# Kernel tuning notes

Measured on AMD Instinct MI355X. Metric: run time of the kernel, lower is better.

The kernel has to match this reference:

```python
import jax, jax.numpy as jnp
import numpy as np

RADIUS = 0.08
NSAMPLE = 32


def setup_inputs() -> dict:
    key = jax.random.key(0)
    k1, k2, k3 = jax.random.split(key, 3)
    xyz = jax.random.uniform(k1, (20000, 3), dtype=jnp.float32)          # (N, 3)
    new_xyz = jax.random.uniform(k2, (2, 2048, 3), dtype=jnp.float32)    # (B, P, 3)
    features = jax.random.normal(k3, (64, 20000), dtype=jnp.float32)     # (C, N)
    return {"xyz": xyz, "new_xyz": new_xyz, "features": features}


def _ball_query(xyz, new_xyz, radius, nsample):
    """Replicates pointnet2 grid ball query.
    Returns idx (B,P,nsample) int32 of the FIRST nsample in-ball point indices
    (in original point order), padded with the first found index (0 if none),
    and idn (B,P,nsample) int32 validity flags (all ones if ball is empty,
    matching the kernel's untouched init of 1).
    """
    xyz = jax.lax.stop_gradient(xyz)
    new_xyz = jax.lax.stop_gradient(new_xyz)
    N = xyz.shape[0]
    # squared distances (B, P, N) via ||a||^2 + ||b||^2 - 2 a.b (no (B,P,N,3) temp)
    x2 = jnp.sum(xyz * xyz, axis=-1)                 # (N,)
    q2 = jnp.sum(new_xyz * new_xyz, axis=-1)         # (B, P)
    cross = jnp.einsum("bpd,nd->bpn", new_xyz, xyz)  # (B, P, N)
    d2 = q2[..., None] + x2[None, None, :] - 2.0 * cross
    mask = d2 < radius * radius                      # (B, P, N)
    # encode "first nsample in-ball indices in ascending point order":
    scores = jnp.where(mask, jnp.arange(N, dtype=jnp.int32), N)
    neg_vals, _ = jax.lax.top_k(-scores, nsample)    # largest of -scores = smallest scores
    cand = -neg_vals                                 # (B, P, nsample), sorted ascending
    valid = cand < N
    first = jnp.where(valid[..., :1], cand[..., :1], 0)
    idx = jnp.where(valid, cand, first).astype(jnp.int32)
    empty = ~valid[..., :1]                          # ball has no neighbors
    idn = jnp.where(valid | empty, 1, 0).astype(jnp.int32)
    return idx, idn


def _group(features, idx):
    """features (C, N), idx (B, P, S) -> (B, C, P, S) gather."""
    g = jnp.take(features, idx, axis=1)              # (C, B, P, S)
    return jnp.transpose(g, (1, 0, 2, 3))


def reference(xyz, new_xyz, features):
    idx, idn = _ball_query(xyz, new_xyz, RADIUS, NSAMPLE)
    grouped_xyz = _group(jnp.transpose(xyz), idx)                    # (B, 3, P, S)
    grouped_xyz = grouped_xyz - jnp.transpose(new_xyz, (0, 2, 1))[..., None]
    grouped_features = _group(features, idx)                         # (B, C, P, S)
    new_features = jnp.concatenate([grouped_xyz, grouped_features], axis=1)
    return new_features, idn
```

## Files before the change

### kernel.cpp

```cpp
#include <hip/hip_runtime.h>
#include <hip/hip_bf16.h>

#define NPTS   20000
#define BATCH  2
#define NQ     2048
#define NS     32
#define NC     64
#define NCOUT  67
#define NQTOT  (BATCH * NQ)
#define NF_ELEMS (BATCH * NCOUT * NQ * NS)

#define GRID   12
#define NCELL  (GRID * GRID * GRID)
#define CAND_CAP 128

__device__ __forceinline__ float sq3(float a, float b, float c) {
    return __fadd_rn(__fadd_rn(__fmul_rn(a, a), __fmul_rn(b, b)), __fmul_rn(c, c));
}

__global__ __launch_bounds__(256) void zero_counts_kernel(int* __restrict__ cnt) {
    const int t = threadIdx.x;
    #pragma unroll
    for (int i = 0; i < 7; ++i) {
        const int c = t * 7 + i;
        if (c < NCELL) cnt[c] = 0;
    }
}

__global__ __launch_bounds__(256) void cell_count_kernel(
        const float* __restrict__ xyz, int* __restrict__ cellOf,
        int* __restrict__ cnt) {
    const int n = blockIdx.x * 256 + threadIdx.x;
    if (n >= NPTS) return;
    const float x = xyz[n * 3 + 0];
    const float y = xyz[n * 3 + 1];
    const float z = xyz[n * 3 + 2];
    const int cx = min(max((int)(x * (float)GRID), 0), GRID - 1);
    const int cy = min(max((int)(y * (float)GRID), 0), GRID - 1);
    const int cz = min(max((int)(z * (float)GRID), 0), GRID - 1);
    const int cell = (cx * GRID + cy) * GRID + cz;
    cellOf[n] = cell;
    atomicAdd(&cnt[cell], 1);
}

__global__ __launch_bounds__(256) void scan_kernel(
        const int* __restrict__ cnt, int* __restrict__ start,
        int* __restrict__ cursor) {
    __shared__ int s[256];
    const int t = threadIdx.x;
    int loc[7];
    int sum = 0;
    #pragma unroll
    for (int i = 0; i < 7; ++i) {
        const int c = t * 7 + i;
        const int v = (c < NCELL) ? cnt[c] : 0;
        loc[i] = sum;
        sum += v;
    }
    s[t] = sum;
    __syncthreads();
    for (int off = 1; off < 256; off <<= 1) {
        const int v = (t >= off) ? s[t - off] : 0;
        __syncthreads();
        s[t] += v;
        __syncthreads();
    }
    const int excl = s[t] - sum;
    #pragma unroll
    for (int i = 0; i < 7; ++i) {
        const int c = t * 7 + i;
        if (c < NCELL) {
            const int val = excl + loc[i];
            start[c]  = val;
            cursor[c] = val;
        }
    }
    if (t == 255) start[NCELL] = s[255];
}

__global__ __launch_bounds__(256) void scatter_kernel(
        const float* __restrict__ xyz, const int* __restrict__ cellOf,
        int* __restrict__ cursor, float4* __restrict__ packed) {
    const int n = blockIdx.x * 256 + threadIdx.x;
    if (n >= NPTS) return;
    const int pos = atomicAdd(&cursor[cellOf[n]], 1);
    packed[pos] = make_float4(xyz[n * 3 + 0], xyz[n * 3 + 1], xyz[n * 3 + 2],
                              __int_as_float(n));
}

__device__ __forceinline__ void ce_shfl(int& r0, int& r1, int j,
                                        bool asc0, bool asc1, int lane) {
    const int o0 = __shfl_xor(r0, j);
    const int o1 = __shfl_xor(r1, j);
    const bool lower = (lane & j) == 0;
    r0 = (lower == asc0) ? min(r0, o0) : max(r0, o0);
    r1 = (lower == asc1) ? min(r1, o1) : max(r1, o1);
}

__global__ __launch_bounds__(256) void grid_query_kernel(
        const float4* __restrict__ packed,
        const int*    __restrict__ cellStart,
        const float*  __restrict__ new_xyz,
        int*   __restrict__ idxOut,
        float* __restrict__ idnOut) {
    const float R2 = (float)(0.08 * 0.08);

    const int wid  = threadIdx.x >> 6;
    const int lane = threadIdx.x & 63;
    const int q    = blockIdx.x * 4 + wid;

    __shared__ int cand[4][CAND_CAP];

    const float qx = new_xyz[q * 3 + 0];
    const float qy = new_xyz[q * 3 + 1];
    const float qz = new_xyz[q * 3 + 2];
    const float q2 = sq3(qx, qy, qz);

    const int cx = min(max((int)(qx * (float)GRID), 0), GRID - 1);
    const int cy = min(max((int)(qy * (float)GRID), 0), GRID - 1);
    const int cz = min(max((int)(qz * (float)GRID), 0), GRID - 1);

    const int xlo = max(cx - 1, 0), xhi = min(cx + 1, GRID - 1);
    const int ylo = max(cy - 1, 0), yhi = min(cy + 1, GRID - 1);
    const int zlo = max(cz - 1, 0), zhi = min(cz + 1, GRID - 1);

    const unsigned long long lt = (1ull << lane) - 1ull;
    int cnt = 0;

    for (int dx = xlo; dx <= xhi; ++dx) {
        for (int dy = ylo; dy <= yhi; ++dy) {
            const int row = (dx * GRID + dy) * GRID;
            const int s0 = cellStart[row + zlo];
            const int s1 = cellStart[row + zhi + 1];
            for (int base = s0; base < s1; base += 64) {
                const int i = base + lane;
                bool inball = false;
                int  pid = 0;
                if (i < s1) {
                    const float4 p = packed[i];
                    pid = __float_as_int(p.w);
                    const float x2 = sq3(p.x, p.y, p.z);
                    const float cross = __fadd_rn(
                        __fadd_rn(__fmul_rn(qx, p.x), __fmul_rn(qy, p.y)),
                        __fmul_rn(qz, p.z));
                    const float d2 = __fsub_rn(__fadd_rn(q2, x2),
                                               __fmul_rn(2.0f, cross));
                    inball = d2 < R2;
                }
                const unsigned long long m = __ballot(inball);
                if (inball) {
                    const int pos = cnt + __popcll(m & lt);
                    if (pos < CAND_CAP) cand[wid][pos] = pid;
                }
                cnt += __popcll(m);
            }
        }
    }

    __threadfence_block();

    const int M = min(cnt, CAND_CAP);
    int r0 = (lane      < M) ? cand[wid][lane]      : 0x7fffffff;
    int r1 = (lane + 64 < M) ? cand[wid][lane + 64] : 0x7fffffff;

    #pragma unroll
    for (int k = 2; k <= 64; k <<= 1) {
        #pragma unroll
        for (int j = k >> 1; j >= 1; j >>= 1) {
            const bool asc0 = ((lane & k) == 0);
            const bool asc1 = (((lane | 64) & k) == 0);
            ce_shfl(r0, r1, j, asc0, asc1, lane);
        }
    }
    { const int lo = min(r0, r1), hi = max(r0, r1); r0 = lo; r1 = hi; }
    #pragma unroll
    for (int j = 32; j >= 1; j >>= 1) ce_shfl(r0, r1, j, true, true, lane);

    const int nf = min(cnt, NS);
    const int first = __shfl(r0, 0);
    if (lane < NS) {
        int v; float fl;
        if (cnt == 0) { v = 0; fl = 1.0f; }
        else { v = (lane < nf) ? r0 : first; fl = (lane < nf) ? 1.0f : 0.0f; }
        idxOut[q * NS + lane] = v;
        idnOut[q * NS + lane] = fl;
    }
}

__global__ __launch_bounds__(256) void ball_query_kernel(
        const float* __restrict__ xyz, const float* __restrict__ new_xyz,
        int* __restrict__ idxOut, float* __restrict__ idnOut) {
    const float R2 = (float)(0.08 * 0.08);
    const int wid  = threadIdx.x >> 6;
    const int lane = threadIdx.x & 63;
    const int q    = blockIdx.x * 4 + wid;
    __shared__ int buf[4][NS];
    const float qx = new_xyz[q * 3 + 0];
    const float qy = new_xyz[q * 3 + 1];
    const float qz = new_xyz[q * 3 + 2];
    const float q2 = sq3(qx, qy, qz);
    int cnt = 0;
    for (int base = 0; base < NPTS; base += 64) {
        const int i = base + lane;
        bool inball = false;
        if (i < NPTS) {
            const float px = xyz[i * 3 + 0], py = xyz[i * 3 + 1], pz = xyz[i * 3 + 2];
            const float x2 = sq3(px, py, pz);
            const float cross = __fadd_rn(
                __fadd_rn(__fmul_rn(qx, px), __fmul_rn(qy, py)), __fmul_rn(qz, pz));
            const float d2 = __fsub_rn(__fadd_rn(q2, x2), __fmul_rn(2.0f, cross));
            inball = d2 < R2;
        }
        const unsigned long long m = __ballot(inball);
        if (inball) {
            const int pos = cnt + __popcll(m & ((1ull << lane) - 1ull));
            if (pos < NS) buf[wid][pos] = i;
        }
        cnt += __popcll(m);
        if (cnt >= NS) break;
    }
    __syncthreads();
    if (lane < NS) {
        const int nf = (cnt < NS) ? cnt : NS;
        int v; float fl;
        if (nf == 0) { v = 0; fl = 1.0f; }
        else { v = (lane < nf) ? buf[wid][lane] : buf[wid][0];
               fl = (lane < nf) ? 1.0f : 0.0f; }
        idxOut[q * NS + lane] = v;
        idnOut[q * NS + lane] = fl;
    }
}

__global__ void feat_transpose_kernel(const float* __restrict__ features,
                                      float* __restrict__ featT) {
    __shared__ float tile[64][65];
    const int n0 = blockIdx.x * 64;
    const int t  = threadIdx.x;
    const int nn   = t & 63;
    const int cgrp = t >> 6;
    for (int k = 0; k < 16; ++k) {
        const int cc = cgrp * 16 + k;
        const int n  = n0 + nn;
        if (n < NPTS) tile[cc][nn] = features[cc * NPTS + n];
    }
    __syncthreads();
    const int cc2  = t & 63;
    const int ngrp = t >> 6;
    for (int k = 0; k < 16; ++k) {
        const int nn2 = ngrp * 16 + k;
        const int n   = n0 + nn2;
        if (n < NPTS) featT[n * NC + cc2] = tile[cc2][nn2];
    }
}

__global__ __launch_bounds__(256) void group_kernel(
        const float* __restrict__ xyz,
        const float* __restrict__ new_xyz,
        const float* __restrict__ features,
        const float* __restrict__ featT,
        const int*   __restrict__ idx,
        float* __restrict__ out,
        int haveFeatT) {
    const int q = blockIdx.x;
    const int b = q >> 11;
    const int p = q & (NQ - 1);

    __shared__ int   sidx[NS];
    __shared__ float sq[3];

    const int t = threadIdx.x;
    if (t < NS) sidx[t] = idx[q * NS + t];
    if (t < 3)  sq[t]   = new_xyz[q * 3 + t];
    __syncthreads();

    if (t < 96) {
        const int d = t >> 5;
        const int s = t & 31;
        const int id = sidx[s];
        const int o = ((b * NCOUT + d) * NQ + p) * NS + s;
        out[o] = __fsub_rn(xyz[id * 3 + d], sq[d]);
    }

    const int s  = t & 31;
    const int c4 = t >> 5;
    const int id = sidx[s];
    const int CH_STRIDE = NQ * NS;

    if (haveFeatT) {
        const float4* ft = (const float4*)featT;
        #pragma unroll
        for (int h = 0; h < 2; ++h) {
            const int cc4 = c4 + h * 8;
            const float4 v = ft[id * (NC / 4) + cc4];
            const int cbase = cc4 * 4;
            const int o = ((b * NCOUT + 3 + cbase) * NQ + p) * NS + s;
            out[o]                 = v.x;
            out[o + 1 * CH_STRIDE] = v.y;
            out[o + 2 * CH_STRIDE] = v.z;
            out[o + 3 * CH_STRIDE] = v.w;
        }
    } else {
        #pragma unroll
        for (int h = 0; h < 2; ++h) {
            const int cbase = (c4 + h * 8) * 4;
            #pragma unroll
            for (int k = 0; k < 4; ++k) {
                const int c = cbase + k;
                const int o = ((b * NCOUT + 3 + c) * NQ + p) * NS + s;
                out[o] = features[c * NPTS + id];
            }
        }
    }
}

extern "C" void kernel_launch(void* const* d_in, const int* in_sizes, int n_in,
                              void* d_out, int out_size, void* d_ws, size_t ws_size,
                              hipStream_t stream) {
    const float* xyz      = (const float*)d_in[0];
    const float* new_xyz  = (const float*)d_in[1];
    const float* features = (const float*)d_in[2];

    float* out     = (float*)d_out;
    float* idn_out = out + NF_ELEMS;

    const size_t OFF_IDX    = 0;
    const size_t OFF_FEATT  = 524288;
    const size_t OFF_CNT    = 5644288;
    const size_t OFF_START  = 5651456;
    const size_t OFF_CURSOR = 5658624;
    const size_t OFF_CELLOF = 5665792;
    const size_t OFF_PACKED = 5745792;
    const size_t GRID_TOTAL = 6065792;
    const size_t FEATT_END  = 5644288;

    int*    d_idx    = (int*)((char*)d_ws + OFF_IDX);
    float*  d_featT  = (float*)((char*)d_ws + OFF_FEATT);
    int*    d_cnt    = (int*)((char*)d_ws + OFF_CNT);
    int*    d_start  = (int*)((char*)d_ws + OFF_START);
    int*    d_cursor = (int*)((char*)d_ws + OFF_CURSOR);
    int*    d_cellOf = (int*)((char*)d_ws + OFF_CELLOF);
    float4* d_packed = (float4*)((char*)d_ws + OFF_PACKED);

    const int haveGrid  = (ws_size >= GRID_TOTAL) ? 1 : 0;
    const int haveFeatT = (ws_size >= FEATT_END) ? 1 : 0;

    if (haveFeatT) {
        feat_transpose_kernel<<<(NPTS + 63) / 64, 256, 0, stream>>>(features, d_featT);
    }

    if (haveGrid) {
        zero_counts_kernel<<<1, 256, 0, stream>>>(d_cnt);
        cell_count_kernel<<<(NPTS + 255) / 256, 256, 0, stream>>>(xyz, d_cellOf, d_cnt);
        scan_kernel<<<1, 256, 0, stream>>>(d_cnt, d_start, d_cursor);
        scatter_kernel<<<(NPTS + 255) / 256, 256, 0, stream>>>(xyz, d_cellOf, d_cursor, d_packed);
        grid_query_kernel<<<NQTOT / 4, 256, 0, stream>>>(d_packed, d_start, new_xyz,
                                                         d_idx, idn_out);
    } else {
        ball_query_kernel<<<NQTOT / 4, 256, 0, stream>>>(xyz, new_xyz, d_idx, idn_out);
    }

    group_kernel<<<NQTOT, 256, 0, stream>>>(xyz, new_xyz, features,
                                            haveFeatT ? d_featT : nullptr,
                                            d_idx, out, haveFeatT);
}
```

Before: 107.1 us.

## Fuse grid query with grouping and feature transpose with cell counting

Merges the feature transpose into the cell-count kernel, and merges the grouping gather into the grid query kernel so that neighbor indices stay in shared memory instead of going through global memory. This cuts two kernel launches and the idx round trip. The brute-force and no-workspace fallbacks are removed, so the code now assumes the workspace is large enough. Grouping now runs with one wave per query instead of a 256-thread block per query, which lowers parallelism in the output-write phase.

Measured after the change: 99.98 us. -6.6%, faster.

```diff
diff --git a/kernel.cpp b/kernel.cpp
--- a/kernel.cpp
+++ b/kernel.cpp
@@ -27,20 +27,44 @@
     }
 }
 
-__global__ __launch_bounds__(256) void cell_count_kernel(
-        const float* __restrict__ xyz, int* __restrict__ cellOf,
+__global__ __launch_bounds__(256) void transpose_count_kernel(
+        const float* __restrict__ features, const float* __restrict__ xyz,
+        float* __restrict__ featT, int* __restrict__ cellOf,
         int* __restrict__ cnt) {
-    const int n = blockIdx.x * 256 + threadIdx.x;
-    if (n >= NPTS) return;
-    const float x = xyz[n * 3 + 0];
-    const float y = xyz[n * 3 + 1];
-    const float z = xyz[n * 3 + 2];
-    const int cx = min(max((int)(x * (float)GRID), 0), GRID - 1);
-    const int cy = min(max((int)(y * (float)GRID), 0), GRID - 1);
-    const int cz = min(max((int)(z * (float)GRID), 0), GRID - 1);
-    const int cell = (cx * GRID + cy) * GRID + cz;
-    cellOf[n] = cell;
-    atomicAdd(&cnt[cell], 1);
+    __shared__ float tile[64][65];
+    const int n0 = blockIdx.x * 64;
+    const int t  = threadIdx.x;
+
+    if (t < 64) {
+        const int n = n0 + t;
+        if (n < NPTS) {
+            const float x = xyz[n * 3 + 0];
+            const float y = xyz[n * 3 + 1];
+            const float z = xyz[n * 3 + 2];
+            const int cx = min(max((int)(x * (float)GRID), 0), GRID - 1);
+            const int cy = min(max((int)(y * (float)GRID), 0), GRID - 1);
+            const int cz = min(max((int)(z * (float)GRID), 0), GRID - 1);
+            const int cell = (cx * GRID + cy) * GRID + cz;
+            cellOf[n] = cell;
+            atomicAdd(&cnt[cell], 1);
+        }
+    }
+
+    const int nn   = t & 63;
+    const int cgrp = t >> 6;
+    for (int k = 0; k < 16; ++k) {
+        const int cc = cgrp * 16 + k;
+        const int n  = n0 + nn;
+        if (n < NPTS) tile[cc][nn] = features[cc * NPTS + n];
+    }
+    __syncthreads();
+    const int cc2  = t & 63;
+    const int ngrp = t >> 6;
+    for (int k = 0; k < 16; ++k) {
+        const int nn2 = ngrp * 16 + k;
+        const int n   = n0 + nn2;
+        if (n < NPTS) featT[n * NC + cc2] = tile[cc2][nn2];
+    }
 }
 
 __global__ __launch_bounds__(256) void scan_kernel(
@@ -97,11 +121,13 @@
     r1 = (lower == asc1) ? min(r1, o1) : max(r1, o1);
 }
 
-__global__ __launch_bounds__(256) void grid_query_kernel(
+__global__ __launch_bounds__(256) void query_group_kernel(
         const float4* __restrict__ packed,
         const int*    __restrict__ cellStart,
         const float*  __restrict__ new_xyz,
-        int*   __restrict__ idxOut,
+        const float*  __restrict__ xyz,
+        const float4* __restrict__ featT4,
+        float* __restrict__ out,
         float* __restrict__ idnOut) {
     const float R2 = (float)(0.08 * 0.08);
 
@@ -110,6 +136,7 @@
     const int q    = blockIdx.x * 4 + wid;
 
     __shared__ int cand[4][CAND_CAP];
+    __shared__ int sidx[4][NS];
 
     const float qx = new_xyz[q * 3 + 0];
     const float qy = new_xyz[q * 3 + 1];
@@ -182,134 +209,37 @@
         int v; float fl;
         if (cnt == 0) { v = 0; fl = 1.0f; }
         else { v = (lane < nf) ? r0 : first; fl = (lane < nf) ? 1.0f : 0.0f; }
-        idxOut[q * NS + lane] = v;
+        sidx[wid][lane] = v;
         idnOut[q * NS + lane] = fl;
     }
-}
-
-__global__ __launch_bounds__(256) void ball_query_kernel(
-        const float* __restrict__ xyz, const float* __restrict__ new_xyz,
-        int* __restrict__ idxOut, float* __restrict__ idnOut) {
-    const float R2 = (float)(0.08 * 0.08);
-    const int wid  = threadIdx.x >> 6;
-    const int lane = threadIdx.x & 63;
-    const int q    = blockIdx.x * 4 + wid;
-    __shared__ int buf[4][NS];
-    const float qx = new_xyz[q * 3 + 0];
-    const float qy = new_xyz[q * 3 + 1];
-    const float qz = new_xyz[q * 3 + 2];
-    const float q2 = sq3(qx, qy, qz);
-    int cnt = 0;
-    for (int base = 0; base < NPTS; base += 64) {
-        const int i = base + lane;
-        bool inball = false;
-        if (i < NPTS) {
-            const float px = xyz[i * 3 + 0], py = xyz[i * 3 + 1], pz = xyz[i * 3 + 2];
-            const float x2 = sq3(px, py, pz);
-            const float cross = __fadd_rn(
-                __fadd_rn(__fmul_rn(qx, px), __fmul_rn(qy, py)), __fmul_rn(qz, pz));
-            const float d2 = __fsub_rn(__fadd_rn(q2, x2), __fmul_rn(2.0f, cross));
-            inball = d2 < R2;
-        }
-        const unsigned long long m = __ballot(inball);
-        if (inball) {
-            const int pos = cnt + __popcll(m & ((1ull << lane) - 1ull));
-            if (pos < NS) buf[wid][pos] = i;
-        }
-        cnt += __popcll(m);
-        if (cnt >= NS) break;
-    }
-    __syncthreads();
-    if (lane < NS) {
-        const int nf = (cnt < NS) ? cnt : NS;
-        int v; float fl;
-        if (nf == 0) { v = 0; fl = 1.0f; }
-        else { v = (lane < nf) ? buf[wid][lane] : buf[wid][0];
-               fl = (lane < nf) ? 1.0f : 0.0f; }
-        idxOut[q * NS + lane] = v;
-        idnOut[q * NS + lane] = fl;
-    }
-}
-
-__global__ void feat_transpose_kernel(const float* __restrict__ features,
-                                      float* __restrict__ featT) {
-    __shared__ float tile[64][65];
-    const int n0 = blockIdx.x * 64;
-    const int t  = threadIdx.x;
-    const int nn   = t & 63;
-    const int cgrp = t >> 6;
-    for (int k = 0; k < 16; ++k) {
-        const int cc = cgrp * 16 + k;
-        const int n  = n0 + nn;
-        if (n < NPTS) tile[cc][nn] = features[cc * NPTS + n];
-    }
-    __syncthreads();
-    const int cc2  = t & 63;
-    const int ngrp = t >> 6;
-    for (int k = 0; k < 16; ++k) {
-        const int nn2 = ngrp * 16 + k;
-        const int n   = n0 + nn2;
-        if (n < NPTS) featT[n * NC + cc2] = tile[cc2][nn2];
-    }
-}
-
-__global__ __launch_bounds__(256) void group_kernel(
-        const float* __restrict__ xyz,
-        const float* __restrict__ new_xyz,
-        const float* __restrict__ features,
-        const float* __restrict__ featT,
-        const int*   __restrict__ idx,
-        float* __restrict__ out,
-        int haveFeatT) {
-    const int q = blockIdx.x;
+
+    __threadfence_block();
+
     const int b = q >> 11;
     const int p = q & (NQ - 1);
-
-    __shared__ int   sidx[NS];
-    __shared__ float sq[3];
-
-    const int t = threadIdx.x;
-    if (t < NS) sidx[t] = idx[q * NS + t];
-    if (t < 3)  sq[t]   = new_xyz[q * 3 + t];
-    __syncthreads();
-
-    if (t < 96) {
-        const int d = t >> 5;
-        const int s = t & 31;
-        const int id = sidx[s];
-        const int o = ((b * NCOUT + d) * NQ + p) * NS + s;
-        out[o] = __fsub_rn(xyz[id * 3 + d], sq[d]);
-    }
-
-    const int s  = t & 31;
-    const int c4 = t >> 5;
-    const int id = sidx[s];
     const int CH_STRIDE = NQ * NS;
 
-    if (haveFeatT) {
-        const float4* ft = (const float4*)featT;
-        #pragma unroll
-        for (int h = 0; h < 2; ++h) {
-            const int cc4 = c4 + h * 8;
-            const float4 v = ft[id * (NC / 4) + cc4];
-            const int cbase = cc4 * 4;
-            const int o = ((b * NCOUT + 3 + cbase) * NQ + p) * NS + s;
-            out[o]                 = v.x;
-            out[o + 1 * CH_STRIDE] = v.y;
-            out[o + 2 * CH_STRIDE] = v.z;
-            out[o + 3 * CH_STRIDE] = v.w;
-        }
-    } else {
-        #pragma unroll
-        for (int h = 0; h < 2; ++h) {
-            const int cbase = (c4 + h * 8) * 4;
-            #pragma unroll
-            for (int k = 0; k < 4; ++k) {
-                const int c = cbase + k;
-                const int o = ((b * NCOUT + 3 + c) * NQ + p) * NS + s;
-                out[o] = features[c * NPTS + id];
-            }
-        }
+    for (int k = lane; k < 96; k += 64) {
+        const int d = k >> 5;
+        const int s = k & 31;
+        const int id = sidx[wid][s];
+        const float qd = (d == 0) ? qx : ((d == 1) ? qy : qz);
+        out[((b * NCOUT + d) * NQ + p) * NS + s] = __fsub_rn(xyz[id * 3 + d], qd);
+    }
+
+    const int s    = lane & 31;
+    const int half = lane >> 5;
+    const int id   = sidx[wid][s];
+    const int rowbase = id * (NC / 4);
+    #pragma unroll
+    for (int k = 0; k < 8; ++k) {
+        const int cc4 = k * 2 + half;
+        const float4 vf = featT4[rowbase + cc4];
+        const int o = ((b * NCOUT + 3 + cc4 * 4) * NQ + p) * NS + s;
+        out[o]                 = vf.x;
+        out[o + 1 * CH_STRIDE] = vf.y;
+        out[o + 2 * CH_STRIDE] = vf.z;
+        out[o + 3 * CH_STRIDE] = vf.w;
     }
 }
 
@@ -323,17 +253,13 @@
     float* out     = (float*)d_out;
     float* idn_out = out + NF_ELEMS;
 
-    const size_t OFF_IDX    = 0;
-    const size_t OFF_FEATT  = 524288;
-    const size_t OFF_CNT    = 5644288;
-    const size_t OFF_START  = 5651456;
-    const size_t OFF_CURSOR = 5658624;
-    const size_t OFF_CELLOF = 5665792;
-    const size_t OFF_PACKED = 5745792;
-    const size_t GRID_TOTAL = 6065792;
-    const size_t FEATT_END  = 5644288;
-
-    int*    d_idx    = (int*)((char*)d_ws + OFF_IDX);
+    const size_t OFF_FEATT  = 0;
+    const size_t OFF_CNT    = 5120000;
+    const size_t OFF_START  = 5127168;
+    const size_t OFF_CURSOR = 5134336;
+    const size_t OFF_CELLOF = 5141504;
+    const size_t OFF_PACKED = 5221504;
+
     float*  d_featT  = (float*)((char*)d_ws + OFF_FEATT);
     int*    d_cnt    = (int*)((char*)d_ws + OFF_CNT);
     int*    d_start  = (int*)((char*)d_ws + OFF_START);
@@ -341,25 +267,12 @@
     int*    d_cellOf = (int*)((char*)d_ws + OFF_CELLOF);
     float4* d_packed = (float4*)((char*)d_ws + OFF_PACKED);
 
-    const int haveGrid  = (ws_size >= GRID_TOTAL) ? 1 : 0;
-    const int haveFeatT = (ws_size >= FEATT_END) ? 1 : 0;
-
-    if (haveFeatT) {
-        feat_transpose_kernel<<<(NPTS + 63) / 64, 256, 0, stream>>>(features, d_featT);
-    }
-
-    if (haveGrid) {
-        zero_counts_kernel<<<1, 256, 0, stream>>>(d_cnt);
-        cell_count_kernel<<<(NPTS + 255) / 256, 256, 0, stream>>>(xyz, d_cellOf, d_cnt);
-        scan_kernel<<<1, 256, 0, stream>>>(d_cnt, d_start, d_cursor);
-        scatter_kernel<<<(NPTS + 255) / 256, 256, 0, stream>>>(xyz, d_cellOf, d_cursor, d_packed);
-        grid_query_kernel<<<NQTOT / 4, 256, 0, stream>>>(d_packed, d_start, new_xyz,
-                                                         d_idx, idn_out);
-    } else {
-        ball_query_kernel<<<NQTOT / 4, 256, 0, stream>>>(xyz, new_xyz, d_idx, idn_out);
-    }
-
-    group_kernel<<<NQTOT, 256, 0, stream>>>(xyz, new_xyz, features,
-                                            haveFeatT ? d_featT : nullptr,
-                                            d_idx, out, haveFeatT);
-}
+    zero_counts_kernel<<<1, 256, 0, stream>>>(d_cnt);
+    transpose_count_kernel<<<(NPTS + 63) / 64, 256, 0, stream>>>(
+        features, xyz, d_featT, d_cellOf, d_cnt);
+    scan_kernel<<<1, 256, 0, stream>>>(d_cnt, d_start, d_cursor);
+    scatter_kernel<<<(NPTS + 255) / 256, 256, 0, stream>>>(
+        xyz, d_cellOf, d_cursor, d_packed);
+    query_group_kernel<<<NQTOT / 4, 256, 0, stream>>>(
+        d_packed, d_start, new_xyz, xyz, (const float4*)d_featT, out, idn_out);
+}
```
